# Kernel optimization log

Hardware: AMD Instinct MI355X
Metric: run time of the kernel (lower is better)

The kernel has to match this reference:

```python
import jax, jax.numpy as jnp
import numpy as np

B, T, NI, NH, NO = 256, 512, 512, 2048, 256

def setup_inputs() -> dict:
    key = jax.random.key(0)
    ks = jax.random.split(key, 7)
    def lin(kw, kb, fan_in, shape_w, shape_b):
        bound = 1.0 / np.sqrt(fan_in)
        W = jax.random.uniform(kw, shape_w, jnp.float32, -bound, bound)
        b = jax.random.uniform(kb, shape_b, jnp.float32, -bound, bound)
        return W, b
    x = jax.random.normal(ks[0], (B, T, NI), jnp.float32)
    W_enc, b_enc = lin(ks[1], ks[2], NI, (NH, NI), (NH,))
    W_rec, b_rec = lin(ks[3], ks[4], NH, (NH, NH), (NH,))
    W_dec, b_dec = lin(ks[5], ks[6], NH, (NO, NH), (NO,))
    dt = jnp.array([0.5], jnp.float32)
    a = jnp.array([1.0], jnp.float32)
    return {"x": x, "dt": dt, "a": a,
            "W_enc": W_enc, "b_enc": b_enc,
            "W_rec": W_rec, "b_rec": b_rec,
            "W_dec": W_dec, "b_dec": b_dec}

def reference(x, dt, a, W_enc, b_enc, W_rec, b_rec, W_dec, b_dec):
    # x: [B, T, NI] -> time-major [T, B, NI]
    s = jax.nn.sigmoid(dt)                      # (1,) gate, broadcasts
    xt = jnp.swapaxes(x, 0, 1)                  # [T, B, NI]
    # Encoder applied to all timesteps at once (same math as per-step Linear)
    enc = jnp.einsum('tbi,hi->tbh', xt, W_enc) + b_enc  # [T, B, NH]
    h0 = jnp.zeros((x.shape[0], W_rec.shape[0]), x.dtype)  # [B, NH]
    def step(h, e_t):
        h = (1.0 - s) * h + s * a * jnp.tanh(e_t + h @ W_rec.T + b_rec)
        y_t = h @ W_dec.T + b_dec               # [B, NO]
        return h, y_t
    h_final, y = jax.lax.scan(step, h0, enc)    # y: [T, B, NO]
    return y, h_final[None]                     # h: [1, B, NH] as in torch
```

## Files before the change

kernel.cpp:

```cpp
#include <hip/hip_runtime.h>
#include <hip/hip_bf16.h>
#include <math.h>


#define B_   256
#define T_   512
#define NI_  512
#define NH_  2048
#define NO_  256

typedef __bf16 bf16_t;
typedef __bf16 bf16x8 __attribute__((ext_vector_type(8)));
typedef float  f32x4  __attribute__((ext_vector_type(4)));

#define MFMA16(a,b,c) __builtin_amdgcn_mfma_f32_16x16x32_bf16((a),(b),(c),0,0,0)
#define XCC_HWREG_IMM (20 | (31 << 11))

__device__ __forceinline__ void ld_sc0_x4(bf16x8& d, const void* p) {
  asm volatile("global_load_dwordx4 %0, %1, off sc0" : "=v"(d) : "v"(p));
}
__device__ __forceinline__ void ld_sc01_u32(unsigned& d, const void* p) {
  asm volatile("global_load_dword %0, %1, off sc0 sc1" : "=v"(d) : "v"(p));
}
__device__ __forceinline__ void st_sc01_u32(void* p, unsigned v) {
  asm volatile("global_store_dword %0, %1, off sc0 sc1" :: "v"(p), "v"(v));
}
#define WAIT_VM0() do { asm volatile("s_waitcnt vmcnt(0)" ::: "memory"); \
                        __builtin_amdgcn_sched_barrier(0); } while (0)
#define WAIT_VM(n) do { asm volatile("s_waitcnt vmcnt(" #n ")" ::: "memory"); \
                        __builtin_amdgcn_sched_barrier(0); } while (0)

__device__ __forceinline__ void spin_ge(int* p, int tgt) {
  while (__hip_atomic_load(p, __ATOMIC_RELAXED, __HIP_MEMORY_SCOPE_AGENT) < tgt)
    __builtin_amdgcn_s_sleep(2);
}
__device__ __forceinline__ void bump(int* p) {
  __hip_atomic_fetch_add(p, 1, __ATOMIC_RELAXED, __HIP_MEMORY_SCOPE_AGENT);
}

__device__ __forceinline__ int* fA_loc(int* s, int x, int r) { return s + (x*32 + r)*16; }
__device__ __forceinline__ int* fA_mir(int* s, int x, int r) { return s + 4096 + (x*32 + r)*16; }
__device__ __forceinline__ int* fA_pub(int* s, int x, int r) { return s + 8192 + (x*32 + r)*16; }

__global__ __launch_bounds__(256) void k_cvt(const float* __restrict__ src,
                                             bf16_t* __restrict__ dst, int n) {
  int i = blockIdx.x * 256 + threadIdx.x;
  const int stride = gridDim.x * 256;
  for (; i < n; i += stride) dst[i] = (bf16_t)src[i];
}

__device__ __forceinline__ void dec_tile(
    int tid, int side, int rank, int rg,
    const bf16_t* hl, const bf16_t* hm,
    const bf16_t* __restrict__ Wdec, const float* __restrict__ b_dec,
    float* __restrict__ y_out, float* Scr)
{
  const int lane = tid & 63, w = tid >> 6, fl = lane & 15, kg = lane >> 4;
  const int drl = side*32 + (rank >> 4)*16;
  const int dc  = (rank & 15) * 16;
  const bf16_t* hbase = ((w >> 3) == side) ? hl : hm;
  const int kb = (w & 7) * 128;
  bf16x8 hf[4];
  #pragma unroll
  for (int i = 0; i < 4; ++i)
    ld_sc0_x4(hf[i], hbase + (size_t)(drl + fl)*1024 + kb + i*32 + kg*8);
  WAIT_VM0();
  f32x4 d = {0.f, 0.f, 0.f, 0.f};
  #pragma unroll
  for (int i = 0; i < 4; ++i) {
    bf16x8 wf = *reinterpret_cast<const bf16x8*>(
        Wdec + (size_t)(dc + fl)*NH_ + w*128 + i*32 + kg*8);
    d = MFMA16(hf[i], wf, d);
  }
  __syncthreads();
  #pragma unroll
  for (int j = 0; j < 4; ++j) Scr[w*256 + (kg*4 + j)*16 + fl] = d[j];
  __syncthreads();
  if (tid < 256) {
    const int r = tid >> 4, c = tid & 15;
    float s = b_dec[dc + c];
    #pragma unroll
    for (int ww = 0; ww < 16; ++ww) s += Scr[ww*256 + r*16 + c];
    y_out[(size_t)(rg*64 + drl + r)*NO_ + dc + c] = s;
  }
}

__global__ __launch_bounds__(1024, 1) void k_prnn(
    const float* __restrict__ x,
    const float* __restrict__ dt_p, const float* __restrict__ a_p,
    const float* __restrict__ Wrec,
    const bf16_t* __restrict__ Wenc_b, const bf16_t* __restrict__ Wdec_b,
    const float* __restrict__ b_rec, const float* __restrict__ b_enc,
    const float* __restrict__ b_dec,
    bf16_t* __restrict__ hloc, bf16_t* __restrict__ hmir,
    bf16_t* __restrict__ pub, int* __restrict__ sync_,
    float* __restrict__ out)
{
  __shared__ alignas(16) bf16x8 Wl[256 * 32];
  __shared__ alignas(16) float  Scr[6144];
  __shared__ alignas(16) bf16_t Ts[2048];
  __shared__ int sh_xcd, sh_rank;

  const int tid  = threadIdx.x;
  const int lane = tid & 63;
  const int fl   = lane & 15;
  const int kg   = lane >> 4;
  const int w    = tid >> 6;
  const int rt   = w & 3;
  const int kq   = w >> 2;

  if (tid == 0) {
    const int xc = (int)(__builtin_amdgcn_s_getreg(XCC_HWREG_IMM) & 7u);
    int* reg = sync_ + 12288 + xc * 16;
    const int rk = __hip_atomic_fetch_add(reg, 1, __ATOMIC_RELAXED, __HIP_MEMORY_SCOPE_AGENT);
    __hip_atomic_fetch_add(sync_ + 12416, 1, __ATOMIC_RELAXED, __HIP_MEMORY_SCOPE_AGENT);
    spin_ge(sync_ + 12416, 256);
    sh_xcd = xc; sh_rank = rk;
  }
  __syncthreads();
  const int xcd = sh_xcd, rank = sh_rank;
  if (rank >= 32) return;
  const int rg = xcd >> 1, side = xcd & 1;

  bf16_t* hloc_x = hloc + (size_t)xcd * 4 * 65536;
  bf16_t* hmir_x = hmir + (size_t)xcd * 4 * 65536;
  bf16_t* pub_own = pub + (size_t)xcd * 2 * 65536;
  bf16_t* pub_par = pub + (size_t)(xcd ^ 1) * 2 * 65536;

  const float sgate = 1.f / (1.f + expf(-dt_p[0]));
  const float av = a_p[0];
  const float gi = 1.f - sgate;
  const float sav = sgate * av;
  const int colbase = rank * 32;
  const int colg0 = side*1024 + colbase + fl;
  const int colg1 = colg0 + 16;
  const float bias0 = b_rec[colg0] + b_enc[colg0];
  const float bias1 = b_rec[colg1] + b_enc[colg1];
  const bf16_t* we0 = Wenc_b + (size_t)colg0 * NI_;
  const bf16_t* we1 = Wenc_b + (size_t)colg1 * NI_;
  const int lrow = rt*16 + fl;
  const int grow = rg*64 + lrow;

  f32x4 hr0 = {0.f,0.f,0.f,0.f}, hr1 = {0.f,0.f,0.f,0.f};

  {
    const int c = tid >> 5, part = tid & 31;
    const int cglob = side*1024 + colbase + c;
    #pragma unroll
    for (int i = 0; i < 8; ++i) {
      const int g = part*8 + i;
      const float* src = Wrec + (size_t)cglob * NH_ + g*8;
      float4 f0 = reinterpret_cast<const float4*>(src)[0];
      float4 f1 = reinterpret_cast<const float4*>(src)[1];
      bf16x8 w8 = {(bf16_t)f0.x, (bf16_t)f0.y, (bf16_t)f0.z, (bf16_t)f0.w,
                   (bf16_t)f1.x, (bf16_t)f1.y, (bf16_t)f1.z, (bf16_t)f1.w};
      Wl[g*32 + c] = w8;
    }
  }
  __syncthreads();

  #pragma unroll 1
  for (int t = 0; t < T_; ++t) {
    const int slotR = (t + 3) & 3;
    const int slotW = t & 3;
    const int pslot = t & 1;

    if (tid < 32)                    spin_ge(fA_loc(sync_, xcd, tid), t);
    else if (tid >= 64 && tid < 96)  spin_ge(fA_mir(sync_, xcd, tid - 64), t);
    __syncthreads();

    const bf16_t* hl = hloc_x + (size_t)slotR * 65536;
    const bf16_t* hm = hmir_x + (size_t)slotR * 65536;

    f32x4 acc0 = {0.f,0.f,0.f,0.f}, acc1 = {0.f,0.f,0.f,0.f};
    const int kbase = kq * 640;
    if (kq < 3) {
      bf16x8 pa[4];
      auto aptr = [&](int c) -> const bf16_t* {
        const int k = kbase + c*32;
        const bf16_t* b = ((k >> 10) == side) ? hl : hm;
        return b + (size_t)lrow*1024 + (k & 1023) + kg*8;
      };
      ld_sc0_x4(pa[0], aptr(0)); ld_sc0_x4(pa[1], aptr(1));
      ld_sc0_x4(pa[2], aptr(2)); ld_sc0_x4(pa[3], aptr(3));
      #pragma unroll 4
      for (int c = 0; c < 16; ++c) {
        WAIT_VM(3);
        const int gg = kbase/8 + c*4 + kg;
        acc0 = MFMA16(pa[c & 3], Wl[gg*32 + fl], acc0);
        acc1 = MFMA16(pa[c & 3], Wl[gg*32 + 16 + fl], acc1);
        ld_sc0_x4(pa[c & 3], aptr(c + 4));
      }
      #pragma unroll
      for (int c = 16; c < 20; ++c) {
        switch (19 - c) { case 3: WAIT_VM(3); break; case 2: WAIT_VM(2); break;
                          case 1: WAIT_VM(1); break; default: WAIT_VM0(); }
        const int gg = kbase/8 + c*4 + kg;
        acc0 = MFMA16(pa[c & 3], Wl[gg*32 + fl], acc0);
        acc1 = MFMA16(pa[c & 3], Wl[gg*32 + 16 + fl], acc1);
      }
    } else {
      const bf16_t* bh = (1 == side) ? hl : hm;
      bf16x8 pa[4];
      #pragma unroll
      for (int c = 0; c < 4; ++c)
        ld_sc0_x4(pa[c], bh + (size_t)lrow*1024 + ((1920 + c*32) & 1023) + kg*8);
      #pragma unroll
      for (int c = 0; c < 4; ++c) {
        switch (3 - c) { case 3: WAIT_VM(3); break; case 2: WAIT_VM(2); break;
                         case 1: WAIT_VM(1); break; default: WAIT_VM0(); }
        const int gg = 240 + c*4 + kg;
        acc0 = MFMA16(pa[c], Wl[gg*32 + fl], acc0);
        acc1 = MFMA16(pa[c], Wl[gg*32 + 16 + fl], acc1);
      }
      const float* xrow = x + ((size_t)grow * T_ + t) * NI_;
      #pragma unroll 4
      for (int c = 0; c < 16; ++c) {
        const int kp = c*32 + kg*8;
        float4 u = *reinterpret_cast<const float4*>(xrow + kp);
        float4 v = *reinterpret_cast<const float4*>(xrow + kp + 4);
        bf16x8 a = {(bf16_t)u.x, (bf16_t)u.y, (bf16_t)u.z, (bf16_t)u.w,
                    (bf16_t)v.x, (bf16_t)v.y, (bf16_t)v.z, (bf16_t)v.w};
        bf16x8 b0 = *reinterpret_cast<const bf16x8*>(we0 + kp);
        bf16x8 b1 = *reinterpret_cast<const bf16x8*>(we1 + kp);
        acc0 = MFMA16(a, b0, acc0);
        acc1 = MFMA16(a, b1, acc1);
      }
    }

    __syncthreads();
    if (kq != 0) {
      const int base = (kq - 1)*2048 + rt*16*32;
      #pragma unroll
      for (int j = 0; j < 4; ++j) {
        Scr[base + (kg*4 + j)*32 + fl]      = acc0[j];
        Scr[base + (kg*4 + j)*32 + 16 + fl] = acc1[j];
      }
    }
    __syncthreads();
    if (kq == 0) {
      #pragma unroll
      for (int j = 0; j < 4; ++j) {
        const int ri = (rt*16 + kg*4 + j)*32;
        const float v0 = acc0[j] + Scr[ri + fl] + Scr[2048 + ri + fl] + Scr[4096 + ri + fl];
        const float v1 = acc1[j] + Scr[ri + 16 + fl] + Scr[2048 + ri + 16 + fl]
                                 + Scr[4096 + ri + 16 + fl];
        const float o0 = gi*hr0[j] + sav*tanhf(v0 + bias0);
        const float o1 = gi*hr1[j] + sav*tanhf(v1 + bias1);
        hr0[j] = o0; hr1[j] = o1;
        Ts[(rt*16 + kg*4 + j)*32 + fl]      = (bf16_t)o0;
        Ts[(rt*16 + kg*4 + j)*32 + 16 + fl] = (bf16_t)o1;
        if (t == T_ - 1) {
          float* hd = out + (size_t)T_*B_*NO_ + (size_t)(rg*64 + rt*16 + kg*4 + j)*NH_;
          hd[colg0] = o0; hd[colg1] = o1;
        }
      }
    }
    __syncthreads();

    {
      const int r = tid >> 4, q = tid & 15;
      const unsigned dv = *reinterpret_cast<const unsigned*>(&Ts[r*32 + q*2]);
      const int off = r*1024 + colbase + q*2;
      *reinterpret_cast<unsigned*>(hloc_x + (size_t)slotW*65536 + off) = dv;
      st_sc01_u32(pub_own + (size_t)pslot*65536 + off, dv);
      WAIT_VM0();
    }
    __syncthreads();
    if (tid == 0)       bump(fA_loc(sync_, xcd, rank));
    else if (tid == 64) bump(fA_pub(sync_, xcd, rank));

    if (t >= 2)
      dec_tile(tid, side, rank, rg,
               hloc_x + (size_t)((t + 2) & 3)*65536,
               hmir_x + (size_t)((t + 2) & 3)*65536,
               Wdec_b, b_dec, out + (size_t)(t - 2)*B_*NO_, Scr);

    if (tid == 0) spin_ge(fA_pub(sync_, xcd ^ 1, rank), t + 1);
    __syncthreads();
    {
      const int r = tid >> 4, q = tid & 15;
      const int off = r*1024 + colbase + q*2;
      unsigned mv;
      ld_sc01_u32(mv, pub_par + (size_t)pslot*65536 + off);
      WAIT_VM0();
      *reinterpret_cast<unsigned*>(hmir_x + (size_t)slotW*65536 + off) = mv;
    }
    __syncthreads();
    if (tid == 0) bump(fA_mir(sync_, xcd, rank));
  }

  if (tid < 32)                    spin_ge(fA_loc(sync_, xcd, tid), T_);
  else if (tid >= 64 && tid < 96)  spin_ge(fA_mir(sync_, xcd, tid - 64), T_);
  __syncthreads();
  dec_tile(tid, side, rank, rg, hloc_x + (size_t)2*65536, hmir_x + (size_t)2*65536,
           Wdec_b, b_dec, out + (size_t)(T_ - 2)*B_*NO_, Scr);
  dec_tile(tid, side, rank, rg, hloc_x + (size_t)3*65536, hmir_x + (size_t)3*65536,
           Wdec_b, b_dec, out + (size_t)(T_ - 1)*B_*NO_, Scr);
}

extern "C" void kernel_launch(void* const* d_in, const int* in_sizes, int n_in,
                              void* d_out, int out_size, void* d_ws, size_t ws_size,
                              hipStream_t stream) {
  const float* x     = (const float*)d_in[0];
  const float* dt_p  = (const float*)d_in[1];
  const float* a_p   = (const float*)d_in[2];
  const float* W_enc = (const float*)d_in[3];
  const float* b_enc = (const float*)d_in[4];
  const float* W_rec = (const float*)d_in[5];
  const float* b_rec = (const float*)d_in[6];
  const float* W_dec = (const float*)d_in[7];
  const float* b_dec = (const float*)d_in[8];
  float* out = (float*)d_out;

  char* p = (char*)d_ws;
  bf16_t* hloc   = (bf16_t*)p;  p += (size_t)8*4*65536*2;
  bf16_t* hmir   = (bf16_t*)p;  p += (size_t)8*4*65536*2;
  bf16_t* pub    = (bf16_t*)p;  p += (size_t)8*2*65536*2;
  bf16_t* Wenc_b = (bf16_t*)p;  p += (size_t)NH_*NI_*2;
  bf16_t* Wdec_b = (bf16_t*)p;  p += (size_t)NO_*NH_*2;
  int*    sync_  = (int*)p;     p += 16384*4;

  hipMemsetAsync(hloc, 0, (size_t)8*4*65536*2, stream);
  hipMemsetAsync(hmir, 0, (size_t)8*4*65536*2, stream);
  hipMemsetAsync(sync_, 0, 16384*4, stream);

  k_cvt<<<128, 256, 0, stream>>>(W_enc, Wenc_b, NH_ * NI_);
  k_cvt<<<64, 256, 0, stream>>>(W_dec, Wdec_b, NO_ * NH_);

  k_prnn<<<dim3(256), dim3(1024), 0, stream>>>(
      x, dt_p, a_p, W_rec, Wenc_b, Wdec_b, b_rec, b_enc, b_dec,
      hloc, hmir, pub, sync_, out);
}
```

Baseline: 12.99 ms.

## Precompute encoder projection ahead into ring buffer and rebalance recurrent K split

Moves the per-step encoder GEMM (x·W_enc) off the critical recurrence path. Warp group 1 now computes it four steps ahead into a per-block global ring buffer, and the finalizing warps read it back. The recurrent K dimension is split evenly across four warp groups, with per-wave spin waits replacing the block-wide wait. The mirror exchange is moved before the decoder tile and uses 16-byte stores and loads in a contiguous publish layout, and the spin sleep is lengthened. The trade-offs are extra global traffic and a ring-buffer round trip, and the change relies on intra-block ordering for the enc writes.

```diff
diff --git a/kernel.cpp b/kernel.cpp
--- a/kernel.cpp
+++ b/kernel.cpp
@@ -19,11 +19,14 @@
 __device__ __forceinline__ void ld_sc0_x4(bf16x8& d, const void* p) {
   asm volatile("global_load_dwordx4 %0, %1, off sc0" : "=v"(d) : "v"(p));
 }
-__device__ __forceinline__ void ld_sc01_u32(unsigned& d, const void* p) {
-  asm volatile("global_load_dword %0, %1, off sc0 sc1" : "=v"(d) : "v"(p));
-}
-__device__ __forceinline__ void st_sc01_u32(void* p, unsigned v) {
-  asm volatile("global_store_dword %0, %1, off sc0 sc1" :: "v"(p), "v"(v));
+__device__ __forceinline__ void ld_sc0_f4(f32x4& d, const void* p) {
+  asm volatile("global_load_dwordx4 %0, %1, off sc0" : "=v"(d) : "v"(p));
+}
+__device__ __forceinline__ void ld_sc01_x4(bf16x8& d, const void* p) {
+  asm volatile("global_load_dwordx4 %0, %1, off sc0 sc1" : "=v"(d) : "v"(p));
+}
+__device__ __forceinline__ void st_sc01_x4(void* p, bf16x8 v) {
+  asm volatile("global_store_dwordx4 %0, %1, off sc0 sc1" :: "v"(p), "v"(v));
 }
 #define WAIT_VM0() do { asm volatile("s_waitcnt vmcnt(0)" ::: "memory"); \
                         __builtin_amdgcn_sched_barrier(0); } while (0)
@@ -32,7 +35,7 @@
 
 __device__ __forceinline__ void spin_ge(int* p, int tgt) {
   while (__hip_atomic_load(p, __ATOMIC_RELAXED, __HIP_MEMORY_SCOPE_AGENT) < tgt)
-    __builtin_amdgcn_s_sleep(2);
+    __builtin_amdgcn_s_sleep(8);
 }
 __device__ __forceinline__ void bump(int* p) {
   __hip_atomic_fetch_add(p, 1, __ATOMIC_RELAXED, __HIP_MEMORY_SCOPE_AGENT);
@@ -93,8 +96,8 @@
     const float* __restrict__ b_rec, const float* __restrict__ b_enc,
     const float* __restrict__ b_dec,
     bf16_t* __restrict__ hloc, bf16_t* __restrict__ hmir,
-    bf16_t* __restrict__ pub, int* __restrict__ sync_,
-    float* __restrict__ out)
+    bf16_t* __restrict__ pub, float* __restrict__ enc_ring,
+    int* __restrict__ sync_, float* __restrict__ out)
 {
   __shared__ alignas(16) bf16x8 Wl[256 * 32];
   __shared__ alignas(16) float  Scr[6144];
@@ -107,7 +110,7 @@
   const int kg   = lane >> 4;
   const int w    = tid >> 6;
   const int rt   = w & 3;
-  const int kq   = w >> 2;
+  const int kc   = w >> 2;
 
   if (tid == 0) {
     const int xc = (int)(__builtin_amdgcn_s_getreg(XCC_HWREG_IMM) & 7u);
@@ -126,6 +129,7 @@
   bf16_t* hmir_x = hmir + (size_t)xcd * 4 * 65536;
   bf16_t* pub_own = pub + (size_t)xcd * 2 * 65536;
   bf16_t* pub_par = pub + (size_t)(xcd ^ 1) * 2 * 65536;
+  float*  enc_base = enc_ring + (size_t)(xcd * 32 + rank) * 4 * 2048;
 
   const float sgate = 1.f / (1.f + expf(-dt_p[0]));
   const float av = a_p[0];
@@ -143,6 +147,24 @@
 
   f32x4 hr0 = {0.f,0.f,0.f,0.f}, hr1 = {0.f,0.f,0.f,0.f};
 
+  auto enc_compute = [&](int tt, int slot) {
+    f32x4 e0 = {0.f,0.f,0.f,0.f}, e1 = {0.f,0.f,0.f,0.f};
+    const float* xr = x + ((size_t)grow * T_ + tt) * NI_;
+    #pragma unroll 4
+    for (int c = 0; c < 16; ++c) {
+      const int kp = c*32 + kg*8;
+      float4 u = *reinterpret_cast<const float4*>(xr + kp);
+      float4 v = *reinterpret_cast<const float4*>(xr + kp + 4);
+      bf16x8 a = {(bf16_t)u.x, (bf16_t)u.y, (bf16_t)u.z, (bf16_t)u.w,
+                  (bf16_t)v.x, (bf16_t)v.y, (bf16_t)v.z, (bf16_t)v.w};
+      e0 = MFMA16(a, *reinterpret_cast<const bf16x8*>(we0 + kp), e0);
+      e1 = MFMA16(a, *reinterpret_cast<const bf16x8*>(we1 + kp), e1);
+    }
+    float* ep = enc_base + (size_t)slot * 2048 + (rt*64 + lane) * 8;
+    *reinterpret_cast<f32x4*>(ep)     = e0;
+    *reinterpret_cast<f32x4*>(ep + 4) = e1;
+  };
+
   {
     const int c = tid >> 5, part = tid & 31;
     const int cglob = side*1024 + colbase + c;
@@ -158,6 +180,10 @@
     }
   }
   __syncthreads();
+  if (kc == 1) {
+    enc_compute(0, 0); enc_compute(1, 1); enc_compute(2, 2); enc_compute(3, 3);
+  }
+  __syncthreads();
 
   #pragma unroll 1
   for (int t = 0; t < T_; ++t) {
@@ -165,72 +191,37 @@
     const int slotW = t & 3;
     const int pslot = t & 1;
 
-    if (tid < 32)                    spin_ge(fA_loc(sync_, xcd, tid), t);
-    else if (tid >= 64 && tid < 96)  spin_ge(fA_mir(sync_, xcd, tid - 64), t);
-    __syncthreads();
+    if (kc < 2) { if (lane < 32) spin_ge(fA_loc(sync_, xcd, lane), t); }
+    else        { if (lane < 32) spin_ge(fA_mir(sync_, xcd, lane), t); }
 
     const bf16_t* hl = hloc_x + (size_t)slotR * 65536;
     const bf16_t* hm = hmir_x + (size_t)slotR * 65536;
 
     f32x4 acc0 = {0.f,0.f,0.f,0.f}, acc1 = {0.f,0.f,0.f,0.f};
-    const int kbase = kq * 640;
-    if (kq < 3) {
+    {
+      const bf16_t* hbuf = (kc < 2) ? hl : hm;
+      const int gbase = ((kc < 2) ? side*128 : (side^1)*128) + (kc & 1)*64;
+      const bf16_t* arow = hbuf + (size_t)lrow*1024 + (kc & 1)*512 + kg*8;
       bf16x8 pa[4];
-      auto aptr = [&](int c) -> const bf16_t* {
-        const int k = kbase + c*32;
-        const bf16_t* b = ((k >> 10) == side) ? hl : hm;
-        return b + (size_t)lrow*1024 + (k & 1023) + kg*8;
-      };
-      ld_sc0_x4(pa[0], aptr(0)); ld_sc0_x4(pa[1], aptr(1));
-      ld_sc0_x4(pa[2], aptr(2)); ld_sc0_x4(pa[3], aptr(3));
-      #pragma unroll 4
+      ld_sc0_x4(pa[0], arow);       ld_sc0_x4(pa[1], arow + 32);
+      ld_sc0_x4(pa[2], arow + 64);  ld_sc0_x4(pa[3], arow + 96);
+      #pragma unroll
       for (int c = 0; c < 16; ++c) {
-        WAIT_VM(3);
-        const int gg = kbase/8 + c*4 + kg;
+        const int rem = 15 - c;
+        if (rem >= 3)      { WAIT_VM(3); }
+        else if (rem == 2) { WAIT_VM(2); }
+        else if (rem == 1) { WAIT_VM(1); }
+        else               { WAIT_VM0(); }
+        const int gg = gbase + c*4 + kg;
         acc0 = MFMA16(pa[c & 3], Wl[gg*32 + fl], acc0);
         acc1 = MFMA16(pa[c & 3], Wl[gg*32 + 16 + fl], acc1);
-        ld_sc0_x4(pa[c & 3], aptr(c + 4));
+        if (c + 4 < 16) ld_sc0_x4(pa[c & 3], arow + (size_t)(c + 4)*32);
       }
-      #pragma unroll
-      for (int c = 16; c < 20; ++c) {
-        switch (19 - c) { case 3: WAIT_VM(3); break; case 2: WAIT_VM(2); break;
-                          case 1: WAIT_VM(1); break; default: WAIT_VM0(); }
-        const int gg = kbase/8 + c*4 + kg;
-        acc0 = MFMA16(pa[c & 3], Wl[gg*32 + fl], acc0);
-        acc1 = MFMA16(pa[c & 3], Wl[gg*32 + 16 + fl], acc1);
-      }
-    } else {
-      const bf16_t* bh = (1 == side) ? hl : hm;
-      bf16x8 pa[4];
-      #pragma unroll
-      for (int c = 0; c < 4; ++c)
-        ld_sc0_x4(pa[c], bh + (size_t)lrow*1024 + ((1920 + c*32) & 1023) + kg*8);
-      #pragma unroll
-      for (int c = 0; c < 4; ++c) {
-        switch (3 - c) { case 3: WAIT_VM(3); break; case 2: WAIT_VM(2); break;
-                         case 1: WAIT_VM(1); break; default: WAIT_VM0(); }
-        const int gg = 240 + c*4 + kg;
-        acc0 = MFMA16(pa[c], Wl[gg*32 + fl], acc0);
-        acc1 = MFMA16(pa[c], Wl[gg*32 + 16 + fl], acc1);
-      }
-      const float* xrow = x + ((size_t)grow * T_ + t) * NI_;
-      #pragma unroll 4
-      for (int c = 0; c < 16; ++c) {
-        const int kp = c*32 + kg*8;
-        float4 u = *reinterpret_cast<const float4*>(xrow + kp);
-        float4 v = *reinterpret_cast<const float4*>(xrow + kp + 4);
-        bf16x8 a = {(bf16_t)u.x, (bf16_t)u.y, (bf16_t)u.z, (bf16_t)u.w,
-                    (bf16_t)v.x, (bf16_t)v.y, (bf16_t)v.z, (bf16_t)v.w};
-        bf16x8 b0 = *reinterpret_cast<const bf16x8*>(we0 + kp);
-        bf16x8 b1 = *reinterpret_cast<const bf16x8*>(we1 + kp);
-        acc0 = MFMA16(a, b0, acc0);
-        acc1 = MFMA16(a, b1, acc1);
-      }
-    }
-
-    __syncthreads();
-    if (kq != 0) {
-      const int base = (kq - 1)*2048 + rt*16*32;
+    }
+
+    __syncthreads();
+    if (kc != 0) {
+      const int base = (kc - 1)*2048 + rt*16*32;
       #pragma unroll
       for (int j = 0; j < 4; ++j) {
         Scr[base + (kg*4 + j)*32 + fl]      = acc0[j];
@@ -238,13 +229,18 @@
       }
     }
     __syncthreads();
-    if (kq == 0) {
+    if (kc == 0) {
+      f32x4 e0, e1;
+      const float* ep = enc_base + (size_t)(t & 3)*2048 + (rt*64 + lane)*8;
+      ld_sc0_f4(e0, ep); ld_sc0_f4(e1, ep + 4);
+      WAIT_VM0();
       #pragma unroll
       for (int j = 0; j < 4; ++j) {
         const int ri = (rt*16 + kg*4 + j)*32;
-        const float v0 = acc0[j] + Scr[ri + fl] + Scr[2048 + ri + fl] + Scr[4096 + ri + fl];
+        const float v0 = acc0[j] + Scr[ri + fl] + Scr[2048 + ri + fl]
+                                 + Scr[4096 + ri + fl] + e0[j];
         const float v1 = acc1[j] + Scr[ri + 16 + fl] + Scr[2048 + ri + 16 + fl]
-                                 + Scr[4096 + ri + 16 + fl];
+                                 + Scr[4096 + ri + 16 + fl] + e1[j];
         const float o0 = gi*hr0[j] + sav*tanhf(v0 + bias0);
         const float o1 = gi*hr1[j] + sav*tanhf(v1 + bias1);
         hr0[j] = o0; hr1[j] = o1;
@@ -258,17 +254,28 @@
     }
     __syncthreads();
 
-    {
-      const int r = tid >> 4, q = tid & 15;
-      const unsigned dv = *reinterpret_cast<const unsigned*>(&Ts[r*32 + q*2]);
-      const int off = r*1024 + colbase + q*2;
-      *reinterpret_cast<unsigned*>(hloc_x + (size_t)slotW*65536 + off) = dv;
-      st_sc01_u32(pub_own + (size_t)pslot*65536 + off, dv);
+    if (tid < 256) {
+      const int r = tid >> 2, c8 = (tid & 3) * 8;
+      bf16x8 v = *reinterpret_cast<const bf16x8*>(&Ts[r*32 + c8]);
+      *reinterpret_cast<bf16x8*>(hloc_x + (size_t)slotW*65536 + r*1024 + colbase + c8) = v;
+      st_sc01_x4(pub_own + (size_t)pslot*65536 + rank*2048 + tid*8, v);
       WAIT_VM0();
     }
     __syncthreads();
     if (tid == 0)       bump(fA_loc(sync_, xcd, rank));
     else if (tid == 64) bump(fA_pub(sync_, xcd, rank));
+
+    if (tid == 0) spin_ge(fA_pub(sync_, xcd ^ 1, rank), t + 1);
+    __syncthreads();
+    if (tid < 256) {
+      bf16x8 mv;
+      ld_sc01_x4(mv, pub_par + (size_t)pslot*65536 + rank*2048 + tid*8);
+      WAIT_VM0();
+      const int r = tid >> 2, c8 = (tid & 3) * 8;
+      *reinterpret_cast<bf16x8*>(hmir_x + (size_t)slotW*65536 + r*1024 + colbase + c8) = mv;
+    }
+    __syncthreads();
+    if (tid == 0) bump(fA_mir(sync_, xcd, rank));
 
     if (t >= 2)
       dec_tile(tid, side, rank, rg,
@@ -276,18 +283,7 @@
                hmir_x + (size_t)((t + 2) & 3)*65536,
                Wdec_b, b_dec, out + (size_t)(t - 2)*B_*NO_, Scr);
 
-    if (tid == 0) spin_ge(fA_pub(sync_, xcd ^ 1, rank), t + 1);
-    __syncthreads();
-    {
-      const int r = tid >> 4, q = tid & 15;
-      const int off = r*1024 + colbase + q*2;
-      unsigned mv;
-      ld_sc01_u32(mv, pub_par + (size_t)pslot*65536 + off);
-      WAIT_VM0();
-      *reinterpret_cast<unsigned*>(hmir_x + (size_t)slotW*65536 + off) = mv;
-    }
-    __syncthreads();
-    if (tid == 0) bump(fA_mir(sync_, xcd, rank));
+    if (kc == 1 && t + 4 < T_) enc_compute(t + 4, t & 3);
   }
 
   if (tid < 32)                    spin_ge(fA_loc(sync_, xcd, tid), T_);
@@ -319,6 +315,7 @@
   bf16_t* pub    = (bf16_t*)p;  p += (size_t)8*2*65536*2;
   bf16_t* Wenc_b = (bf16_t*)p;  p += (size_t)NH_*NI_*2;
   bf16_t* Wdec_b = (bf16_t*)p;  p += (size_t)NO_*NH_*2;
+  float*  enc    = (float*)p;   p += (size_t)256*4*2048*4;
   int*    sync_  = (int*)p;     p += 16384*4;
 
   hipMemsetAsync(hloc, 0, (size_t)8*4*65536*2, stream);
@@ -330,5 +327,5 @@
 
   k_prnn<<<dim3(256), dim3(1024), 0, stream>>>(
       x, dt_p, a_p, W_rec, Wenc_b, Wdec_b, b_rec, b_enc, b_dec,
-      hloc, hmir, pub, sync_, out);
-}
+      hloc, hmir, pub, enc, sync_, out);
+}
```

New measurement: 13.56 ms. 1.04x slower.
